# Kernel tuning notes

Hardware: AMD Instinct MI355X
Metric: run time of the kernel (lower is better)

The kernel has to match this reference:

```python
import jax, jax.numpy as jnp
import numpy as np

# IntConv2d config
IN_C, OUT_C, K, STRIDE, PAD = 64, 128, 3, 1, 1
BATCH, H, W = 64, 56, 56


def setup_inputs() -> dict:
    key = jax.random.key(0)
    k1, k2 = jax.random.split(key, 2)
    # int8 NHWC activations (values in [-128, 127])
    x = jax.random.randint(k1, (BATCH, H, W, IN_C), -128, 128, dtype=jnp.int32).astype(jnp.int8)
    # weight layout (O, kH, kW, I) exactly as in the torch module
    weight = jax.random.randint(k2, (OUT_C, K, K, IN_C), -128, 128, dtype=jnp.int32).astype(jnp.int8)
    # module initializes bias to zeros(int8)
    bias = jnp.zeros((OUT_C,), dtype=jnp.int8)
    return {"x": x, "weight": weight, "bias": bias}


def reference(x, weight, bias):
    # int8 conv with exact int32 accumulation (what int8conv_cuda computes),
    # NHWC activations, OHWI weights -> NHWC int32 output.
    y = jax.lax.conv_general_dilated(
        x.astype(jnp.int32),
        weight.astype(jnp.int32),
        window_strides=(STRIDE, STRIDE),
        padding=((PAD, PAD), (PAD, PAD)),
        dimension_numbers=("NHWC", "OHWI", "NHWC"),
    )
    # int8 bias broadcast-added over channel dim; promotes to int32
    return y + bias.astype(jnp.int32)
```

## Files before the change

kernel.cpp:

```cpp
#include <hip/hip_runtime.h>

typedef int int4v __attribute__((ext_vector_type(4)));

#define IN_C    64
#define OUT_C   128
#define NPIX    200704
#define KTOT    576
#define N_W     73728
#define N_OUT   25690112

#define PIXB    80

__global__ __launch_bounds__(256) void pack_w_kernel(const int* __restrict__ wgt,
                                                     unsigned int* __restrict__ w8) {
    int t = blockIdx.x * 256 + threadIdx.x;
    int d = t << 2;
    int byte = d & 15;
    int lane = (d >> 4) & 63;
    int ntk  = d >> 10;
    int nt   = ntk & 7;
    int kt   = ntk >> 3;
    int k = kt * 64 + ((lane >> 4) << 4) + byte;
    int n = nt * 16 + (lane & 15);
    int4v v = *(const int4v*)(wgt + n * KTOT + k);
    w8[t] = (v.x & 0xff) | ((v.y & 0xff) << 8) | ((v.z & 0xff) << 16)
          | ((unsigned int)v.w << 24);
}

__global__ __launch_bounds__(256, 4) void conv_halo_kernel(const int* __restrict__ x32,
                                                           const char* __restrict__ w8,
                                                           const int* __restrict__ bias,
                                                           int* __restrict__ out) {
    __shared__ char hx[100 * PIXB];

    const int tid  = threadIdx.x;
    const int lane = tid & 63;
    const int wv   = tid >> 6;
    const int l15  = lane & 15;
    const int l4   = lane >> 4;

    const int bid = blockIdx.x;
    const int nb  = (bid & 7) * 392 + (bid >> 3);

    const int n   = nb / 49;
    const int rr  = nb - n * 49;
    const int th  = rr / 7;
    const int tw  = rr - th * 7;
    const int h0  = th * 8 - 1;
    const int w0  = tw * 8 - 1;

    for (int u = tid; u < 400; u += 256) {
        int pix = u >> 2;
        int q   = u & 3;
        int hr  = pix / 10;
        int hc  = pix - hr * 10;
        int gh  = h0 + hr;
        int gw  = w0 + hc;
        int4v pk = {0, 0, 0, 0};
        if ((unsigned)gh < 56u && (unsigned)gw < 56u) {
            const int4v* src = (const int4v*)x32 + (((n * 56 + gh) * 56 + gw) << 4) + (q << 2);
            int4v a0 = src[0], a1 = src[1], a2 = src[2], a3 = src[3];
            pk.x = (a0.x & 0xff) | ((a0.y & 0xff) << 8) | ((a0.z & 0xff) << 16) | (a0.w << 24);
            pk.y = (a1.x & 0xff) | ((a1.y & 0xff) << 8) | ((a1.z & 0xff) << 16) | (a1.w << 24);
            pk.z = (a2.x & 0xff) | ((a2.y & 0xff) << 8) | ((a2.z & 0xff) << 16) | (a2.w << 24);
            pk.w = (a3.x & 0xff) | ((a3.y & 0xff) << 8) | ((a3.z & 0xff) << 16) | (a3.w << 24);
        }
        *(int4v*)(hx + pix * PIXB + (q << 4)) = pk;
    }
    __syncthreads();

    const char* aptr = hx + ((l15 >> 3) * 10 + (l15 & 7)) * PIXB + (l4 << 4);

    int4v acc[4][2];
#pragma unroll
    for (int mt = 0; mt < 4; ++mt) {
        acc[mt][0] = (int4v){0, 0, 0, 0};
        acc[mt][1] = (int4v){0, 0, 0, 0};
    }

    const char* wp = w8 + (((wv * 2) * 64 + lane) << 4);
    int4v bc0 = *(const int4v*)(wp);
    int4v bc1 = *(const int4v*)(wp + 1024);
    int toff = 0;
#pragma unroll 1
    for (int kt = 0; kt < 9; ++kt) {
        wp += 8192;
        int4v bn0 = *(const int4v*)(wp);
        int4v bn1 = *(const int4v*)(wp + 1024);
#pragma unroll
        for (int mt = 0; mt < 4; ++mt) {
            int4v a = *(const int4v*)(aptr + toff + mt * 1600);
            acc[mt][0] = __builtin_amdgcn_mfma_i32_16x16x64_i8(bc0, a, acc[mt][0], 0, 0, 0);
            acc[mt][1] = __builtin_amdgcn_mfma_i32_16x16x64_i8(bc1, a, acc[mt][1], 0, 0, 0);
        }
        bc0 = bn0;
        bc1 = bn1;
        toff += 80;
        if ((kt == 2) | (kt == 5)) toff += 560;
    }

    const int chb = wv * 32 + (l4 << 2);
    int4v bv0 = *(const int4v*)(bias + chb);
    int4v bv1 = *(const int4v*)(bias + chb + 16);
    int* ob = out + (((n * 56 + th * 8) * 56 + tw * 8) << 7);
    const int pc = l15 & 7;
    const int prl = l15 >> 3;
#pragma unroll
    for (int mt = 0; mt < 4; ++mt) {
        int pr = (mt << 1) + prl;
        int* o = ob + ((pr * 56 + pc) << 7) + chb;
        *(int4v*)(o)      = acc[mt][0] + bv0;
        *(int4v*)(o + 16) = acc[mt][1] + bv1;
    }
}

__global__ __launch_bounds__(256) void conv_naive_kernel(const int* __restrict__ x,
                                                         const int* __restrict__ wgt,
                                                         const int* __restrict__ bias,
                                                         int* __restrict__ out) {
    int idx = blockIdx.x * 256 + threadIdx.x;
    if (idx >= N_OUT) return;
    int ch  = idx & 127;
    int pix = idx >> 7;
    int n  = pix / 3136;
    int r2 = pix - n * 3136;
    int h  = r2 / 56;
    int w  = r2 - h * 56;
    int acc = bias[ch];
    for (int kh = 0; kh < 3; ++kh) {
        int hxr = h + kh - 1;
        if ((unsigned)hxr >= 56u) continue;
        for (int kw = 0; kw < 3; ++kw) {
            int wx = w + kw - 1;
            if ((unsigned)wx >= 56u) continue;
            const int* xp = x + ((n * 56 + hxr) * 56 + wx) * 64;
            const int* wp = wgt + ch * KTOT + (kh * 3 + kw) * 64;
            for (int ic = 0; ic < 64; ++ic) acc += xp[ic] * wp[ic];
        }
    }
    out[idx] = acc;
}

extern "C" void kernel_launch(void* const* d_in, const int* in_sizes, int n_in,
                              void* d_out, int out_size, void* d_ws, size_t ws_size,
                              hipStream_t stream) {
    const int* x    = (const int*)d_in[0];
    const int* wgt  = (const int*)d_in[1];
    const int* bias = (const int*)d_in[2];
    int* out = (int*)d_out;

    if (ws_size >= (size_t)(N_W + 8192)) {
        char* w8 = (char*)d_ws;
        pack_w_kernel<<<N_W / 4 / 256, 256, 0, stream>>>(wgt, (unsigned int*)w8);
        conv_halo_kernel<<<3136, 256, 0, stream>>>(x, w8, bias, out);
    } else {
        conv_naive_kernel<<<(N_OUT + 255) / 256, 256, 0, stream>>>(x, wgt, bias, out);
    }
}
```

Measured before the change: 41.64 us.

## Make conv kernel persistent with double-buffered halo tile prefetch

Replaces the one-tile-per-block launch with 512 persistent blocks, each looping over a contiguous range of 8x8 output tiles. The global loads for the next tile's halo are issued into registers before the current tile's MFMA loop and written to a second LDS buffer afterwards, so load latency can overlap compute. Launch bounds drop to 2 blocks per CU to make room for the extra live registers. The cost is fewer resident waves for hiding latency and an uneven tile split across blocks.

```diff
diff --git a/kernel.cpp b/kernel.cpp
--- a/kernel.cpp
+++ b/kernel.cpp
@@ -4,12 +4,13 @@
 
 #define IN_C    64
 #define OUT_C   128
-#define NPIX    200704
 #define KTOT    576
 #define N_W     73728
 #define N_OUT   25690112
 
 #define PIXB    80
+#define NTILES  3136
+#define NBLK    512
 
 __global__ __launch_bounds__(256) void pack_w_kernel(const int* __restrict__ wgt,
                                                      unsigned int* __restrict__ w8) {
@@ -27,11 +28,15 @@
           | ((unsigned int)v.w << 24);
 }
 
-__global__ __launch_bounds__(256, 4) void conv_halo_kernel(const int* __restrict__ x32,
+__device__ __forceinline__ int pack4(int4v a) {
+    return (a.x & 0xff) | ((a.y & 0xff) << 8) | ((a.z & 0xff) << 16) | (a.w << 24);
+}
+
+__global__ __launch_bounds__(256, 2) void conv_pipe_kernel(const int* __restrict__ x32,
                                                            const char* __restrict__ w8,
                                                            const int* __restrict__ bias,
                                                            int* __restrict__ out) {
-    __shared__ char hx[100 * PIXB];
+    __shared__ char hx[2][100 * PIXB];
 
     const int tid  = threadIdx.x;
     const int lane = tid & 63;
@@ -39,78 +44,112 @@
     const int l15  = lane & 15;
     const int l4   = lane >> 4;
 
-    const int bid = blockIdx.x;
-    const int nb  = (bid & 7) * 392 + (bid >> 3);
+    const int rb = ((blockIdx.x & 7) << 6) + (blockIdx.x >> 3);
+    const int t0 = (rb * NTILES) >> 9;
+    const int t1 = ((rb + 1) * NTILES) >> 9;
 
-    const int n   = nb / 49;
-    const int rr  = nb - n * 49;
-    const int th  = rr / 7;
-    const int tw  = rr - th * 7;
-    const int h0  = th * 8 - 1;
-    const int w0  = tw * 8 - 1;
+    const int pix0 = tid >> 2, q0 = tid & 3;
+    const int hr0 = pix0 / 10, hc0 = pix0 - hr0 * 10;
+    const bool has1 = tid < 144;
+    const int pix1 = (tid + 256) >> 2, q1 = tid & 3;
+    const int hr1 = pix1 / 10, hc1 = pix1 - hr1 * 10;
 
-    for (int u = tid; u < 400; u += 256) {
-        int pix = u >> 2;
-        int q   = u & 3;
-        int hr  = pix / 10;
-        int hc  = pix - hr * 10;
-        int gh  = h0 + hr;
-        int gw  = w0 + hc;
+    const int lanebase = ((l15 >> 3) * 10 + (l15 & 7)) * PIXB + (l4 << 4);
+    const int chb = wv * 32 + (l4 << 2);
+    const int4v bv0 = *(const int4v*)(bias + chb);
+    const int4v bv1 = *(const int4v*)(bias + chb + 16);
+    const int pc = l15 & 7, prl = l15 >> 3;
+    const char* wbase = w8 + (((wv * 2) * 64 + lane) << 4);
+
+    int4v r00, r01, r02, r03, r10, r11, r12, r13;
+    bool ok0 = false, ok1 = false;
+
+    auto load_tile = [&](int t) {
+        int n  = t / 49;
+        int rr = t - n * 49;
+        int th = rr / 7, tw = rr - th * 7;
+        int h0 = th * 8 - 1, w0 = tw * 8 - 1;
+        int gh0 = h0 + hr0, gw0 = w0 + hc0;
+        ok0 = ((unsigned)gh0 < 56u) & ((unsigned)gw0 < 56u);
+        if (ok0) {
+            const int4v* s = (const int4v*)x32 + (((n * 56 + gh0) * 56 + gw0) << 4) + (q0 << 2);
+            r00 = s[0]; r01 = s[1]; r02 = s[2]; r03 = s[3];
+        }
+        if (has1) {
+            int gh1 = h0 + hr1, gw1 = w0 + hc1;
+            ok1 = ((unsigned)gh1 < 56u) & ((unsigned)gw1 < 56u);
+            if (ok1) {
+                const int4v* s = (const int4v*)x32 + (((n * 56 + gh1) * 56 + gw1) << 4) + (q1 << 2);
+                r10 = s[0]; r11 = s[1]; r12 = s[2]; r13 = s[3];
+            }
+        }
+    };
+
+    auto write_tile = [&](int buf) {
         int4v pk = {0, 0, 0, 0};
-        if ((unsigned)gh < 56u && (unsigned)gw < 56u) {
-            const int4v* src = (const int4v*)x32 + (((n * 56 + gh) * 56 + gw) << 4) + (q << 2);
-            int4v a0 = src[0], a1 = src[1], a2 = src[2], a3 = src[3];
-            pk.x = (a0.x & 0xff) | ((a0.y & 0xff) << 8) | ((a0.z & 0xff) << 16) | (a0.w << 24);
-            pk.y = (a1.x & 0xff) | ((a1.y & 0xff) << 8) | ((a1.z & 0xff) << 16) | (a1.w << 24);
-            pk.z = (a2.x & 0xff) | ((a2.y & 0xff) << 8) | ((a2.z & 0xff) << 16) | (a2.w << 24);
-            pk.w = (a3.x & 0xff) | ((a3.y & 0xff) << 8) | ((a3.z & 0xff) << 16) | (a3.w << 24);
+        if (ok0) { pk.x = pack4(r00); pk.y = pack4(r01); pk.z = pack4(r02); pk.w = pack4(r03); }
+        *(int4v*)(hx[buf] + pix0 * PIXB + (q0 << 4)) = pk;
+        if (has1) {
+            int4v pk1 = {0, 0, 0, 0};
+            if (ok1) { pk1.x = pack4(r10); pk1.y = pack4(r11); pk1.z = pack4(r12); pk1.w = pack4(r13); }
+            *(int4v*)(hx[buf] + pix1 * PIXB + (q1 << 4)) = pk1;
         }
-        *(int4v*)(hx + pix * PIXB + (q << 4)) = pk;
-    }
-    __syncthreads();
+    };
 
-    const char* aptr = hx + ((l15 >> 3) * 10 + (l15 & 7)) * PIXB + (l4 << 4);
+    load_tile(t0);
+    write_tile(0);
 
-    int4v acc[4][2];
-#pragma unroll
-    for (int mt = 0; mt < 4; ++mt) {
-        acc[mt][0] = (int4v){0, 0, 0, 0};
-        acc[mt][1] = (int4v){0, 0, 0, 0};
-    }
+    int cur = 0;
+#pragma unroll 1
+    for (int t = t0; t < t1; ++t) {
+        const bool hn = (t + 1) < t1;
+        if (hn) load_tile(t + 1);
+        __syncthreads();
 
-    const char* wp = w8 + (((wv * 2) * 64 + lane) << 4);
-    int4v bc0 = *(const int4v*)(wp);
-    int4v bc1 = *(const int4v*)(wp + 1024);
-    int toff = 0;
-#pragma unroll 1
-    for (int kt = 0; kt < 9; ++kt) {
-        wp += 8192;
-        int4v bn0 = *(const int4v*)(wp);
-        int4v bn1 = *(const int4v*)(wp + 1024);
+        int n  = t / 49;
+        int rr = t - n * 49;
+        int th = rr / 7, tw = rr - th * 7;
+        const char* ap = hx[cur] + lanebase;
+
+        int4v acc[4][2];
 #pragma unroll
         for (int mt = 0; mt < 4; ++mt) {
-            int4v a = *(const int4v*)(aptr + toff + mt * 1600);
-            acc[mt][0] = __builtin_amdgcn_mfma_i32_16x16x64_i8(bc0, a, acc[mt][0], 0, 0, 0);
-            acc[mt][1] = __builtin_amdgcn_mfma_i32_16x16x64_i8(bc1, a, acc[mt][1], 0, 0, 0);
+            acc[mt][0] = (int4v){0, 0, 0, 0};
+            acc[mt][1] = (int4v){0, 0, 0, 0};
         }
-        bc0 = bn0;
-        bc1 = bn1;
-        toff += 80;
-        if ((kt == 2) | (kt == 5)) toff += 560;
-    }
 
-    const int chb = wv * 32 + (l4 << 2);
-    int4v bv0 = *(const int4v*)(bias + chb);
-    int4v bv1 = *(const int4v*)(bias + chb + 16);
-    int* ob = out + (((n * 56 + th * 8) * 56 + tw * 8) << 7);
-    const int pc = l15 & 7;
-    const int prl = l15 >> 3;
+        const char* wp = wbase;
+        int4v bc0 = *(const int4v*)(wp);
+        int4v bc1 = *(const int4v*)(wp + 1024);
+        int toff = 0;
+#pragma unroll 1
+        for (int kt = 0; kt < 9; ++kt) {
+            wp += 8192;
+            int4v bn0 = *(const int4v*)(wp);
+            int4v bn1 = *(const int4v*)(wp + 1024);
 #pragma unroll
-    for (int mt = 0; mt < 4; ++mt) {
-        int pr = (mt << 1) + prl;
-        int* o = ob + ((pr * 56 + pc) << 7) + chb;
-        *(int4v*)(o)      = acc[mt][0] + bv0;
-        *(int4v*)(o + 16) = acc[mt][1] + bv1;
+            for (int mt = 0; mt < 4; ++mt) {
+                int4v a = *(const int4v*)(ap + toff + mt * 1600);
+                acc[mt][0] = __builtin_amdgcn_mfma_i32_16x16x64_i8(bc0, a, acc[mt][0], 0, 0, 0);
+                acc[mt][1] = __builtin_amdgcn_mfma_i32_16x16x64_i8(bc1, a, acc[mt][1], 0, 0, 0);
+            }
+            bc0 = bn0;
+            bc1 = bn1;
+            toff += 80;
+            if ((kt == 2) | (kt == 5)) toff += 560;
+        }
+
+        int* ob = out + (((n * 56 + th * 8) * 56 + tw * 8) << 7);
+#pragma unroll
+        for (int mt = 0; mt < 4; ++mt) {
+            int pr = (mt << 1) + prl;
+            int* o = ob + ((pr * 56 + pc) << 7) + chb;
+            *(int4v*)(o)      = acc[mt][0] + bv0;
+            *(int4v*)(o + 16) = acc[mt][1] + bv1;
+        }
+
+        if (hn) write_tile(cur ^ 1);
+        cur ^= 1;
     }
 }
 
@@ -152,7 +191,7 @@
     if (ws_size >= (size_t)(N_W + 8192)) {
         char* w8 = (char*)d_ws;
         pack_w_kernel<<<N_W / 4 / 256, 256, 0, stream>>>(wgt, (unsigned int*)w8);
-        conv_halo_kernel<<<3136, 256, 0, stream>>>(x, w8, bias, out);
+        conv_pipe_kernel<<<NBLK, 256, 0, stream>>>(x, w8, bias, out);
     } else {
         conv_naive_kernel<<<(N_OUT + 255) / 256, 256, 0, stream>>>(x, wgt, bias, out);
     }
```

Result: slower. 49.72 us (+19.4%).
